# Kernel optimization log

Measured on AMD Instinct MI355X. Metric: run time of the kernel, lower is better.

Reference implementation:

```python
import jax, jax.numpy as jnp
import numpy as np

IN_SIZE = 64
RES = 1024
B = 16
T = 2048
ALPHA = 0.5
SPECTRAL_RADIUS = 0.9


def setup_inputs() -> dict:
    key = jax.random.key(0)
    ks = jax.random.split(key, 8)
    # W_hh scaled so spectral radius ~ SPECTRAL_RADIUS (circular law: |eig|max ~ sqrt(R)*std)
    scale_hh = SPECTRAL_RADIUS / np.sqrt(RES)
    return {
        "x": jax.random.normal(ks[0], (B, T, IN_SIZE), dtype=jnp.float32),
        "W_in0": jax.random.normal(ks[1], (IN_SIZE, RES), dtype=jnp.float32) * 0.5,
        "W_hh0": jax.random.normal(ks[2], (RES, RES), dtype=jnp.float32) * scale_hh,
        "b0": jax.random.normal(ks[3], (1, RES), dtype=jnp.float32) * 0.5,
        "W_in1": jax.random.normal(ks[4], (RES, RES), dtype=jnp.float32) * 0.1,
        "W_hh1": jax.random.normal(ks[5], (RES, RES), dtype=jnp.float32) * scale_hh,
        "b1": jax.random.normal(ks[6], (1, RES), dtype=jnp.float32) * 0.5,
        "readout": jax.random.normal(ks[7], (2 * RES, IN_SIZE), dtype=jnp.float32) * 0.02,
    }


def _reservoir_layer(xs, W_in, W_hh, b, alpha):
    # xs: [T, B, F] time-major; sequential leaky-integrator scan over T
    h0 = jnp.zeros((xs.shape[1], W_hh.shape[0]), dtype=xs.dtype)

    def step(h, x_i):
        h = (1.0 - alpha) * h + alpha * jnp.tanh(x_i @ W_in + h @ W_hh + b)
        return h, h

    _, states = jax.lax.scan(step, h0, xs)
    return states  # [T, B, R]


def reference(x, W_in0, W_hh0, b0, W_in1, W_hh1, b1, readout):
    xt = jnp.transpose(x, (1, 0, 2))  # [T, B, in]
    s0 = _reservoir_layer(xt, W_in0, W_hh0, b0, ALPHA)  # [T, B, R]
    s1 = _reservoir_layer(s0, W_in1, W_hh1, b1, ALPHA)  # [T, B, R]
    h = jnp.concatenate([s0, s1], axis=-1)  # [T, B, 2R]
    out = h @ readout  # [T, B, in]
    return jnp.transpose(out, (1, 0, 2))  # [B, T, in]
```

## Files before the change

### kernel.cpp

```cpp
#include <hip/hip_runtime.h>
#include <math.h>

#define ESN_B 16
#define ESN_T 2048
#define ESN_R 1024
#define ESN_IN 64
#define NBR (ESN_B * ESN_R)

#define OFF_WT_HH0 0
#define OFF_WT_IN1 (1024 * 1024)
#define OFF_WT_HH1 (2 * 1024 * 1024)
#define OFF_WT_IN0 (3 * 1024 * 1024)
#define OFF_RT     (OFF_WT_IN0 + 1024 * 64)
#define OFF_S0G    (OFF_RT + 64 * 2048)
#define OFF_S1G    (OFF_S0G + 2 * NBR)
#define OFF_FLAGS  (OFF_S1G + 2 * NBR)

typedef float vfloat4 __attribute__((__vector_size__(16)));

__global__ void __launch_bounds__(256) transpose_k(const float* __restrict__ src,
                                                   float* __restrict__ dst,
                                                   int rows, int cols) {
  __shared__ float tile[32][33];
  int bx = blockIdx.x * 32, by = blockIdx.y * 32;
  int tx = threadIdx.x, ty = threadIdx.y;
  #pragma unroll
  for (int i = ty; i < 32; i += 8) {
    int r = by + i, c = bx + tx;
    if (r < rows && c < cols) tile[i][tx] = src[(size_t)r * cols + c];
  }
  __syncthreads();
  #pragma unroll
  for (int i = ty; i < 32; i += 8) {
    int c = bx + i, r = by + tx;
    if (c < cols && r < rows) dst[(size_t)c * rows + r] = tile[tx][i];
  }
}

__device__ __forceinline__ float fast_tanh(float v) {
  float a = fabsf(v);
  float e = __expf(-2.0f * a);
  float t = __fdividef(1.0f - e, 1.0f + e);
  return copysignf(t, v);
}

__device__ __forceinline__ float dot4(float4 a, float4 b, float acc) {
  acc = fmaf(a.x, b.x, acc);
  acc = fmaf(a.y, b.y, acc);
  acc = fmaf(a.z, b.z, acc);
  acc = fmaf(a.w, b.w, acc);
  return acc;
}

__device__ __forceinline__ float wave_red64(float v) {
  #pragma unroll
  for (int off = 32; off > 0; off >>= 1) v += __shfl_xor(v, off, 64);
  return v;
}

__device__ __forceinline__ float reduce4(float a0, float a1, float a2, float a3,
                                         bool lb0, bool lb1) {
  float uA = lb0 ? a0 : a1, kA = lb0 ? a1 : a0;
  float A = kA + __shfl_xor(uA, 1, 64);
  float uB = lb0 ? a2 : a3, kB = lb0 ? a3 : a2;
  float B = kB + __shfl_xor(uB, 1, 64);
  float uC = lb1 ? A : B, kC = lb1 ? B : A;
  float C = kC + __shfl_xor(uC, 2, 64);
  C += __shfl_xor(C, 4, 64);
  C += __shfl_xor(C, 8, 64);
  C += __shfl_xor(C, 16, 64);
  C += __shfl_xor(C, 32, 64);
  return C;
}

__device__ __forceinline__ void llc_store_f32x4(float* p, float4 v) {
  vfloat4 vv = {v.x, v.y, v.z, v.w};
  asm volatile("global_store_dwordx4 %0, %1, off sc1" :: "v"(p), "v"(vv) : "memory");
}
__device__ __forceinline__ void llc_store_u32(unsigned* p, unsigned v) {
  asm volatile("global_store_dword %0, %1, off sc1" :: "v"(p), "v"(v) : "memory");
}
__device__ __forceinline__ unsigned llc_load_u32(const unsigned* p) {
  unsigned f;
  asm volatile("global_load_dword %0, %1, off sc1\n\ts_waitcnt vmcnt(0)"
               : "=v"(f) : "v"(p) : "memory");
  return f;
}
__device__ __forceinline__ void vmcnt0() {
  asm volatile("s_waitcnt vmcnt(0)" ::: "memory");
}
__device__ __forceinline__ void barrier_only() {
  asm volatile("" ::: "memory");
  __builtin_amdgcn_s_barrier();
  asm volatile("" ::: "memory");
}
__device__ __forceinline__ void barrier_lgkm() {
  asm volatile("s_waitcnt lgkmcnt(0)" ::: "memory");
  __builtin_amdgcn_s_barrier();
  asm volatile("" ::: "memory");
}

__global__ void __launch_bounds__(512, 2) esn_scan_kernel(
    const float* __restrict__ x,
    const float* __restrict__ b0,
    const float* __restrict__ b1,
    float* __restrict__ wsf,
    float* __restrict__ out) {
  __shared__ float s0l[2][4][1024];
  __shared__ float s1l[4][1024];
  __shared__ __align__(16) float res[2][4][16];
  extern __shared__ float dyn_pad[];
  if (blockIdx.x == 0x7fffffffu) dyn_pad[0] = 1.0f;

  const float* wtHH0 = wsf + OFF_WT_HH0;
  const float* wtIN1 = wsf + OFF_WT_IN1;
  const float* wtHH1 = wsf + OFF_WT_HH1;
  const float* wtIN0 = wsf + OFF_WT_IN0;
  const float* rt    = wsf + OFF_RT;
  float* s0g = wsf + OFF_S0G;
  float* s1g = wsf + OFF_S1G;
  unsigned* flags = (unsigned*)(wsf + OFF_FLAGS);

  const int tid = threadIdx.x;
  const int l = tid & 63;
  const int w = tid >> 6;
  const int bid = blockIdx.x;
  const int g = bid >> 6;
  const int bg = bid & 63;
  const int batch0 = g * 4;
  const int wg = bg * 8 + w;
  const int c0 = wg * 2;
  const int wl2 = w * 2;
  const bool doRO = (w >= 4);
  const int rbl = w - 4;
  const int rb = batch0 + rbl;
  const int roc = bg;
  unsigned* gflags = flags + g * 64;
  const bool lb0 = (l & 1) != 0;
  const bool lb1 = (l & 2) != 0;

  float4 wA0_0, wA0_1, wA0_2, wA0_3, wA1_0, wA1_1, wA1_2, wA1_3;
  float4 wB0_0, wB0_1, wB0_2, wB0_3, wB1_0, wB1_1, wB1_2, wB1_3;
  float4 wC0_0, wC0_1, wC0_2, wC0_3, wC1_0, wC1_1, wC1_2, wC1_3;
  float4 rd0, rd1, rd2, rd3, rd4, rd5, rd6, rd7;

#define LOADW(cc) { \
    const float* pA = wtHH0 + (size_t)(c0 + cc) * ESN_R + l * 4; \
    const float* pB = wtIN1 + (size_t)(c0 + cc) * ESN_R + l * 4; \
    const float* pC = wtHH1 + (size_t)(c0 + cc) * ESN_R + l * 4; \
    wA##cc##_0 = *(const float4*)(pA);       wA##cc##_1 = *(const float4*)(pA + 256); \
    wA##cc##_2 = *(const float4*)(pA + 512); wA##cc##_3 = *(const float4*)(pA + 768); \
    wB##cc##_0 = *(const float4*)(pB);       wB##cc##_1 = *(const float4*)(pB + 256); \
    wB##cc##_2 = *(const float4*)(pB + 512); wB##cc##_3 = *(const float4*)(pB + 768); \
    wC##cc##_0 = *(const float4*)(pC);       wC##cc##_1 = *(const float4*)(pC + 256); \
    wC##cc##_2 = *(const float4*)(pC + 512); wC##cc##_3 = *(const float4*)(pC + 768); \
  }
  LOADW(0) LOADW(1)
#undef LOADW

  rd0 = rd1 = rd2 = rd3 = rd4 = rd5 = rd6 = rd7 = make_float4(0.f, 0.f, 0.f, 0.f);
  if (doRO) {
    const float* pr = rt + (size_t)roc * 2048 + l * 4;
    rd0 = *(const float4*)(pr);        rd1 = *(const float4*)(pr + 256);
    rd2 = *(const float4*)(pr + 512);  rd3 = *(const float4*)(pr + 768);
    rd4 = *(const float4*)(pr + 1024); rd5 = *(const float4*)(pr + 1280);
    rd6 = *(const float4*)(pr + 1536); rd7 = *(const float4*)(pr + 1792);
  }
  const float wI0 = wtIN0[(size_t)(c0 + 0) * ESN_IN + l];
  const float wI1 = wtIN0[(size_t)(c0 + 1) * ESN_IN + l];
  float bsel = 0.f;
  if (l < 4) bsel = ((l < 2) ? b0 : b1)[c0 + (l & 1)];

  const float* sA0 = s0g + 0 * NBR + batch0 * ESN_R + tid * 4;
  const float* sA1 = s0g + 1 * NBR + batch0 * ESN_R + tid * 4;
  const float* sB0 = s1g + 0 * NBR + batch0 * ESN_R + tid * 4;
  const float* sB1 = s1g + 1 * NBR + batch0 * ESN_R + tid * 4;
  float* gb = ((l < 16) ? s0g : s1g) +
              (batch0 + ((l >> 2) & 3)) * ESN_R + bg * 16 + (l & 3) * 4;
  float* gbA = gb;
  float* gbB = gb + NBR;
  const float* xbase = x + (size_t)batch0 * ESN_T * ESN_IN + l;

#define ESN_ROUND(SLOTC, rr)                                                   \
  {                                                                            \
    const bool doL0 = ((rr) < ESN_T);                                          \
    const bool doL1 = ((rr) >= 1 && (rr) <= ESN_T);                            \
    float xv0 = 0.f, xv1 = 0.f, xv2 = 0.f, xv3 = 0.f;                          \
    if (doL0) {                                                                \
      const float* xp = xbase + (size_t)(rr) * ESN_IN;                         \
      xv0 = xp[0 * ESN_T * ESN_IN];                                            \
      xv1 = xp[1 * ESN_T * ESN_IN];                                            \
      xv2 = xp[2 * ESN_T * ESN_IN];                                            \
      xv3 = xp[3 * ESN_T * ESN_IN];                                            \
    }                                                                          \
    if ((rr) > 0) {                                                            \
      if (w == 0) {                                                            \
        while (!__all(llc_load_u32(&gflags[l]) >= (unsigned)(rr))) {}          \
      }                                                                        \
      barrier_only();            \
    }                                                                          \
    const float* p0 = SLOTC ? sA0 : sA1;        \
    const float* p1 = SLOTC ? sB0 : sB1;                                       \
    float4 t0, t1, u0, u1;                                                     \
    asm volatile(                                                              \
        "global_load_dwordx4 %0, %4, off sc1\n\t"                              \
        "global_load_dwordx4 %1, %5, off sc1\n\t"                              \
        "global_load_dwordx4 %2, %6, off sc1\n\t"                              \
        "global_load_dwordx4 %3, %7, off sc1\n\t"                              \
        "s_waitcnt vmcnt(0)"                                                   \
        : "=&v"(t0), "=&v"(t1), "=&v"(u0), "=&v"(u1)                           \
        : "v"(p0), "v"(p0 + 2048), "v"(p1), "v"(p1 + 2048)                     \
        : "memory");                                                           \
    {                                                                          \
      float* d0 = &s0l[SLOTC][0][0] + tid * 4;                                 \
      float* d1 = &s1l[0][0] + tid * 4;                                        \
      *(float4*)(d0)        = t0;                                              \
      *(float4*)(d0 + 2048) = t1;                                              \
      *(float4*)(d1)        = u0;                                              \
      *(float4*)(d1 + 2048) = u1;                                              \
    }                                                                          \
    barrier_lgkm();                                \
    _Pragma("unroll")                                                          \
    for (int bb = 0; bb < 4; ++bb) {                                           \
      const float* hp = &s0l[SLOTC][bb][l * 4];                                \
      float4 h0x = *(const float4*)(hp);                                       \
      float4 h1x = *(const float4*)(hp + 256);                                 \
      float4 h2x = *(const float4*)(hp + 512);                                 \
      float4 h3x = *(const float4*)(hp + 768);                                 \
      const float* gp = &s1l[bb][l * 4];                                       \
      float4 g0x = *(const float4*)(gp);                                       \
      float4 g1x = *(const float4*)(gp + 256);                                 \
      float4 g2x = *(const float4*)(gp + 512);                                 \
      float4 g3x = *(const float4*)(gp + 768);                                 \
      float xb = (bb == 0) ? xv0 : (bb == 1) ? xv1 : (bb == 2) ? xv2 : xv3;    \
      float a0 = xb * wI0, a1 = xb * wI1;                                      \
      a0 = dot4(wA0_0, h0x, a0); a0 = dot4(wA0_1, h1x, a0);                    \
      a0 = dot4(wA0_2, h2x, a0); a0 = dot4(wA0_3, h3x, a0);                    \
      a1 = dot4(wA1_0, h0x, a1); a1 = dot4(wA1_1, h1x, a1);                    \
      a1 = dot4(wA1_2, h2x, a1); a1 = dot4(wA1_3, h3x, a1);                    \
      float a2 = 0.f, a3 = 0.f;                                                \
      a2 = dot4(wB0_0, h0x, a2); a2 = dot4(wB0_1, h1x, a2);                    \
      a2 = dot4(wB0_2, h2x, a2); a2 = dot4(wB0_3, h3x, a2);                    \
      a2 = dot4(wC0_0, g0x, a2); a2 = dot4(wC0_1, g1x, a2);                    \
      a2 = dot4(wC0_2, g2x, a2); a2 = dot4(wC0_3, g3x, a2);                    \
      a3 = dot4(wB1_0, h0x, a3); a3 = dot4(wB1_1, h1x, a3);                    \
      a3 = dot4(wB1_2, h2x, a3); a3 = dot4(wB1_3, h3x, a3);                    \
      a3 = dot4(wC1_0, g0x, a3); a3 = dot4(wC1_1, g1x, a3);                    \
      a3 = dot4(wC1_2, g2x, a3); a3 = dot4(wC1_3, g3x, a3);                    \
      float C = reduce4(a0, a1, a2, a3, lb0, lb1);                             \
      if (l < 4) {                 \
        const float* pbase = (l < 2) ? &s0l[SLOTC][bb][0] : &s1l[bb][0];       \
        float prev = pbase[c0 + (l & 1)];                                      \
        float nv = 0.5f * prev + 0.5f * fast_tanh(C + bsel);                   \
        bool wr = (l < 2) ? doL0 : doL1;                                       \
        if (wr) res[l >> 1][bb][wl2 + (l & 1)] = nv;                           \
      }                                                                        \
    }                                                                          \
    barrier_lgkm();                                      \
    if (w == 0) {                                                              \
      if (l < 32 && ((l < 16) ? doL0 : doL1)) {                                \
        float4 v = *(const float4*)&res[l >> 4][(l >> 2) & 3][(l & 3) * 4];    \
        llc_store_f32x4(SLOTC ? gbB : gbA, v);                                 \
      }                                                                        \
      vmcnt0();                                                                \
      if (l == 0) llc_store_u32(&gflags[bg], (unsigned)((rr) + 1));            \
    }                                                                          \
    if ((rr) >= 2 && doRO) {                                                   \
      const float* sp = &s0l[1 - SLOTC][rbl][l * 4];                           \
      const float* tp = &s1l[rbl][l * 4];                                      \
      float a = 0.f;                                                           \
      a = dot4(rd0, *(const float4*)(sp), a);                                  \
      a = dot4(rd1, *(const float4*)(sp + 256), a);                            \
      a = dot4(rd2, *(const float4*)(sp + 512), a);                            \
      a = dot4(rd3, *(const float4*)(sp + 768), a);                            \
      a = dot4(rd4, *(const float4*)(tp), a);                                  \
      a = dot4(rd5, *(const float4*)(tp + 256), a);                            \
      a = dot4(rd6, *(const float4*)(tp + 512), a);                            \
      a = dot4(rd7, *(const float4*)(tp + 768), a);                            \
      a = wave_red64(a);                                                       \
      if (l == 0) out[((size_t)rb * ESN_T + ((rr) - 2)) * ESN_IN + roc] = a;   \
    }                                                                          \
  }

  for (int rp = 0; rp < (ESN_T + 2) / 2; ++rp) {
    const int r0 = rp * 2;
    ESN_ROUND(0, r0)
    ESN_ROUND(1, r0 + 1)
  }
#undef ESN_ROUND
}

extern "C" void kernel_launch(void* const* d_in, const int* in_sizes, int n_in,
                              void* d_out, int out_size, void* d_ws, size_t ws_size,
                              hipStream_t stream) {
  (void)in_sizes; (void)n_in; (void)out_size; (void)ws_size;
  const float* x     = (const float*)d_in[0];
  const float* w_in0 = (const float*)d_in[1];
  const float* w_hh0 = (const float*)d_in[2];
  const float* b0    = (const float*)d_in[3];
  const float* w_in1 = (const float*)d_in[4];
  const float* w_hh1 = (const float*)d_in[5];
  const float* b1    = (const float*)d_in[6];
  const float* rdo   = (const float*)d_in[7];
  float* out = (float*)d_out;
  float* wsf = (float*)d_ws;

  dim3 tb(32, 8);
  transpose_k<<<dim3(32, 32), tb, 0, stream>>>(w_hh0, wsf + OFF_WT_HH0, 1024, 1024);
  transpose_k<<<dim3(32, 32), tb, 0, stream>>>(w_in1, wsf + OFF_WT_IN1, 1024, 1024);
  transpose_k<<<dim3(32, 32), tb, 0, stream>>>(w_hh1, wsf + OFF_WT_HH1, 1024, 1024);
  transpose_k<<<dim3(32, 2),  tb, 0, stream>>>(w_in0, wsf + OFF_WT_IN0, 64, 1024);
  transpose_k<<<dim3(2, 64),  tb, 0, stream>>>(rdo,   wsf + OFF_RT, 2048, 64);

  (void)hipMemsetAsync(wsf + OFF_S0G + NBR, 0, NBR * sizeof(float), stream);
  (void)hipMemsetAsync(wsf + OFF_S1G, 0, 2 * NBR * sizeof(float), stream);
  (void)hipMemsetAsync(wsf + OFF_FLAGS, 0, 4 * 64 * sizeof(unsigned), stream);

  esn_scan_kernel<<<dim3(256), dim3(512), 40960, stream>>>(x, b0, b1, wsf, out);
}
```

Before: 11.48 ms.

## Triple-buffer layer-0 LDS state so every wave polls flags and one barrier is dropped

```diff
diff --git a/kernel.cpp b/kernel.cpp
--- a/kernel.cpp
+++ b/kernel.cpp
@@ -89,11 +89,6 @@
 __device__ __forceinline__ void vmcnt0() {
   asm volatile("s_waitcnt vmcnt(0)" ::: "memory");
 }
-__device__ __forceinline__ void barrier_only() {
-  asm volatile("" ::: "memory");
-  __builtin_amdgcn_s_barrier();
-  asm volatile("" ::: "memory");
-}
 __device__ __forceinline__ void barrier_lgkm() {
   asm volatile("s_waitcnt lgkmcnt(0)" ::: "memory");
   __builtin_amdgcn_s_barrier();
@@ -106,11 +101,9 @@
     const float* __restrict__ b1,
     float* __restrict__ wsf,
     float* __restrict__ out) {
-  __shared__ float s0l[2][4][1024];
-  __shared__ float s1l[4][1024];
-  __shared__ __align__(16) float res[2][4][16];
-  extern __shared__ float dyn_pad[];
-  if (blockIdx.x == 0x7fffffffu) dyn_pad[0] = 1.0f;
+  __shared__ float s0l[3][4][1024];
+  __shared__ float s1l[2][4][1024];
+  __shared__ __align__(16) float res[2][4][20];
 
   const float* wtHH0 = wsf + OFF_WT_HH0;
   const float* wtIN1 = wsf + OFF_WT_IN1;
@@ -131,7 +124,7 @@
   const int wg = bg * 8 + w;
   const int c0 = wg * 2;
   const int wl2 = w * 2;
-  const bool doRO = (w >= 4);
+  const bool doROw = (w >= 4);
   const int rbl = w - 4;
   const int rb = batch0 + rbl;
   const int roc = bg;
@@ -159,7 +152,7 @@
 #undef LOADW
 
   rd0 = rd1 = rd2 = rd3 = rd4 = rd5 = rd6 = rd7 = make_float4(0.f, 0.f, 0.f, 0.f);
-  if (doRO) {
+  if (doROw) {
     const float* pr = rt + (size_t)roc * 2048 + l * 4;
     rd0 = *(const float4*)(pr);        rd1 = *(const float4*)(pr + 256);
     rd2 = *(const float4*)(pr + 512);  rd3 = *(const float4*)(pr + 768);
@@ -181,10 +174,11 @@
   float* gbB = gb + NBR;
   const float* xbase = x + (size_t)batch0 * ESN_T * ESN_IN + l;
 
-#define ESN_ROUND(SLOTC, rr)                                                   \
+#define ESN_ROUND(S0S, PAR, rr)                                                \
   {                                                                            \
     const bool doL0 = ((rr) < ESN_T);                                          \
     const bool doL1 = ((rr) >= 1 && (rr) <= ESN_T);                            \
+    const bool doRO = ((rr) >= 2 && (rr) < ESN_T + 2) && doROw;                \
     float xv0 = 0.f, xv1 = 0.f, xv2 = 0.f, xv3 = 0.f;                          \
     if (doL0) {                                                                \
       const float* xp = xbase + (size_t)(rr) * ESN_IN;                         \
@@ -193,14 +187,11 @@
       xv2 = xp[2 * ESN_T * ESN_IN];                                            \
       xv3 = xp[3 * ESN_T * ESN_IN];                                            \
     }                                                                          \
-    if ((rr) > 0) {                                                            \
-      if (w == 0) {                                                            \
-        while (!__all(llc_load_u32(&gflags[l]) >= (unsigned)(rr))) {}          \
-      }                                                                        \
-      barrier_only();            \
-    }                                                                          \
-    const float* p0 = SLOTC ? sA0 : sA1;        \
-    const float* p1 = SLOTC ? sB0 : sB1;                                       \
+    if ((rr) > 0) {             \
+      while (!__all(llc_load_u32(&gflags[l]) >= (unsigned)(rr))) {}            \
+    }                                                                          \
+    const float* p0 = (PAR) ? sA0 : sA1;      \
+    const float* p1 = (PAR) ? sB0 : sB1;                                       \
     float4 t0, t1, u0, u1;                                                     \
     asm volatile(                                                              \
         "global_load_dwordx4 %0, %4, off sc1\n\t"                              \
@@ -212,22 +203,22 @@
         : "v"(p0), "v"(p0 + 2048), "v"(p1), "v"(p1 + 2048)                     \
         : "memory");                                                           \
     {                                                                          \
-      float* d0 = &s0l[SLOTC][0][0] + tid * 4;                                 \
-      float* d1 = &s1l[0][0] + tid * 4;                                        \
+      float* d0 = &s0l[S0S][0][0] + tid * 4;                                   \
+      float* d1 = &s1l[PAR][0][0] + tid * 4;                                   \
       *(float4*)(d0)        = t0;                                              \
       *(float4*)(d0 + 2048) = t1;                                              \
       *(float4*)(d1)        = u0;                                              \
       *(float4*)(d1 + 2048) = u1;                                              \
     }                                                                          \
-    barrier_lgkm();                                \
+    barrier_lgkm();                     \
     _Pragma("unroll")                                                          \
     for (int bb = 0; bb < 4; ++bb) {                                           \
-      const float* hp = &s0l[SLOTC][bb][l * 4];                                \
+      const float* hp = &s0l[S0S][bb][l * 4];                                  \
       float4 h0x = *(const float4*)(hp);                                       \
       float4 h1x = *(const float4*)(hp + 256);                                 \
       float4 h2x = *(const float4*)(hp + 512);                                 \
       float4 h3x = *(const float4*)(hp + 768);                                 \
-      const float* gp = &s1l[bb][l * 4];                                       \
+      const float* gp = &s1l[PAR][bb][l * 4];                                  \
       float4 g0x = *(const float4*)(gp);                                       \
       float4 g1x = *(const float4*)(gp + 256);                                 \
       float4 g2x = *(const float4*)(gp + 512);                                 \
@@ -249,7 +240,7 @@
       a3 = dot4(wC1_2, g2x, a3); a3 = dot4(wC1_3, g3x, a3);                    \
       float C = reduce4(a0, a1, a2, a3, lb0, lb1);                             \
       if (l < 4) {                 \
-        const float* pbase = (l < 2) ? &s0l[SLOTC][bb][0] : &s1l[bb][0];       \
+        const float* pbase = (l < 2) ? &s0l[S0S][bb][0] : &s1l[PAR][bb][0];    \
         float prev = pbase[c0 + (l & 1)];                                      \
         float nv = 0.5f * prev + 0.5f * fast_tanh(C + bsel);                   \
         bool wr = (l < 2) ? doL0 : doL1;                                       \
@@ -259,15 +250,19 @@
     barrier_lgkm();                                      \
     if (w == 0) {                                                              \
       if (l < 32 && ((l < 16) ? doL0 : doL1)) {                                \
-        float4 v = *(const float4*)&res[l >> 4][(l >> 2) & 3][(l & 3) * 4];    \
-        llc_store_f32x4(SLOTC ? gbB : gbA, v);                                 \
+        float4 v;                                                              \
+        {                                                                      \
+          const float* rp_ = &res[l >> 4][(l >> 2) & 3][(l & 3) * 4];          \
+          v = *(const float4*)rp_;                                             \
+        }                                                                      \
+        llc_store_f32x4((PAR) ? gbB : gbA, v);                                 \
       }                                                                        \
       vmcnt0();                                                                \
       if (l == 0) llc_store_u32(&gflags[bg], (unsigned)((rr) + 1));            \
     }                                                                          \
-    if ((rr) >= 2 && doRO) {                                                   \
-      const float* sp = &s0l[1 - SLOTC][rbl][l * 4];                           \
-      const float* tp = &s1l[rbl][l * 4];                                      \
+    if (doRO) {   \
+      const float* sp = &s0l[(S0S + 2) % 3][rbl][l * 4];                       \
+      const float* tp = &s1l[PAR][rbl][l * 4];                                 \
       float a = 0.f;                                                           \
       a = dot4(rd0, *(const float4*)(sp), a);                                  \
       a = dot4(rd1, *(const float4*)(sp + 256), a);                            \
@@ -282,10 +277,14 @@
     }                                                                          \
   }
 
-  for (int rp = 0; rp < (ESN_T + 2) / 2; ++rp) {
-    const int r0 = rp * 2;
-    ESN_ROUND(0, r0)
-    ESN_ROUND(1, r0 + 1)
+  for (int rp = 0; rp < 342; ++rp) {
+    const int r0 = rp * 6;
+    ESN_ROUND(0, 0, r0 + 0)
+    ESN_ROUND(1, 1, r0 + 1)
+    ESN_ROUND(2, 0, r0 + 2)
+    ESN_ROUND(0, 1, r0 + 3)
+    ESN_ROUND(1, 0, r0 + 4)
+    ESN_ROUND(2, 1, r0 + 5)
   }
 #undef ESN_ROUND
 }
@@ -316,5 +315,5 @@
   (void)hipMemsetAsync(wsf + OFF_S1G, 0, 2 * NBR * sizeof(float), stream);
   (void)hipMemsetAsync(wsf + OFF_FLAGS, 0, 4 * 64 * sizeof(unsigned), stream);
 
-  esn_scan_kernel<<<dim3(256), dim3(512), 40960, stream>>>(x, b0, b1, wsf, out);
-}
+  esn_scan_kernel<<<dim3(256), dim3(512), 0, stream>>>(x, b0, b1, wsf, out);
+}
```

Measured after the change: 14.55 ms. +26.8%, slower.

## Publish per-wave state and flags directly, dropping block-level staging barrier

Applied to the files above, without the earlier changes.

```diff
diff --git a/kernel.cpp b/kernel.cpp
--- a/kernel.cpp
+++ b/kernel.cpp
@@ -6,6 +6,7 @@
 #define ESN_R 1024
 #define ESN_IN 64
 #define NBR (ESN_B * ESN_R)
+#define SLOTF 16384
 
 #define OFF_WT_HH0 0
 #define OFF_WT_IN1 (1024 * 1024)
@@ -13,8 +14,8 @@
 #define OFF_WT_IN0 (3 * 1024 * 1024)
 #define OFF_RT     (OFF_WT_IN0 + 1024 * 64)
 #define OFF_S0G    (OFF_RT + 64 * 2048)
-#define OFF_S1G    (OFF_S0G + 2 * NBR)
-#define OFF_FLAGS  (OFF_S1G + 2 * NBR)
+#define OFF_S1G    (OFF_S0G + 2 * SLOTF)
+#define OFF_FLAGS  (OFF_S1G + 2 * SLOTF)
 
 typedef float vfloat4 __attribute__((__vector_size__(16)));
 
@@ -73,18 +74,8 @@
   return C;
 }
 
-__device__ __forceinline__ void llc_store_f32x4(float* p, float4 v) {
-  vfloat4 vv = {v.x, v.y, v.z, v.w};
-  asm volatile("global_store_dwordx4 %0, %1, off sc1" :: "v"(p), "v"(vv) : "memory");
-}
 __device__ __forceinline__ void llc_store_u32(unsigned* p, unsigned v) {
   asm volatile("global_store_dword %0, %1, off sc1" :: "v"(p), "v"(v) : "memory");
-}
-__device__ __forceinline__ unsigned llc_load_u32(const unsigned* p) {
-  unsigned f;
-  asm volatile("global_load_dword %0, %1, off sc1\n\ts_waitcnt vmcnt(0)"
-               : "=v"(f) : "v"(p) : "memory");
-  return f;
 }
 __device__ __forceinline__ void vmcnt0() {
   asm volatile("s_waitcnt vmcnt(0)" ::: "memory");
@@ -108,7 +99,6 @@
     float* __restrict__ out) {
   __shared__ float s0l[2][4][1024];
   __shared__ float s1l[4][1024];
-  __shared__ __align__(16) float res[2][4][16];
   extern __shared__ float dyn_pad[];
   if (blockIdx.x == 0x7fffffffu) dyn_pad[0] = 1.0f;
 
@@ -130,12 +120,12 @@
   const int batch0 = g * 4;
   const int wg = bg * 8 + w;
   const int c0 = wg * 2;
-  const int wl2 = w * 2;
-  const bool doRO = (w >= 4);
+  const bool doROw = (w >= 4);
   const int rbl = w - 4;
   const int rb = batch0 + rbl;
   const int roc = bg;
-  unsigned* gflags = flags + g * 64;
+  unsigned* gflags = flags + g * 512;
+  unsigned* myflag = gflags + bg * 8 + w;
   const bool lb0 = (l & 1) != 0;
   const bool lb1 = (l & 2) != 0;
 
@@ -159,7 +149,7 @@
 #undef LOADW
 
   rd0 = rd1 = rd2 = rd3 = rd4 = rd5 = rd6 = rd7 = make_float4(0.f, 0.f, 0.f, 0.f);
-  if (doRO) {
+  if (doROw) {
     const float* pr = rt + (size_t)roc * 2048 + l * 4;
     rd0 = *(const float4*)(pr);        rd1 = *(const float4*)(pr + 256);
     rd2 = *(const float4*)(pr + 512);  rd3 = *(const float4*)(pr + 768);
@@ -171,20 +161,20 @@
   float bsel = 0.f;
   if (l < 4) bsel = ((l < 2) ? b0 : b1)[c0 + (l & 1)];
 
-  const float* sA0 = s0g + 0 * NBR + batch0 * ESN_R + tid * 4;
-  const float* sA1 = s0g + 1 * NBR + batch0 * ESN_R + tid * 4;
-  const float* sB0 = s1g + 0 * NBR + batch0 * ESN_R + tid * 4;
-  const float* sB1 = s1g + 1 * NBR + batch0 * ESN_R + tid * 4;
-  float* gb = ((l < 16) ? s0g : s1g) +
-              (batch0 + ((l >> 2) & 3)) * ESN_R + bg * 16 + (l & 3) * 4;
-  float* gbA = gb;
-  float* gbB = gb + NBR;
+  const float* sA0 = s0g + 0 * SLOTF + g * 4096 + tid * 4;
+  const float* sA1 = s0g + 1 * SLOTF + g * 4096 + tid * 4;
+  const float* sB0 = s1g + 0 * SLOTF + g * 4096 + tid * 4;
+  const float* sB1 = s1g + 1 * SLOTF + g * 4096 + tid * 4;
+  float* stv = ((l < 2) ? s0g : s1g) + g * 4096 + (c0 + (l & 1)) * 4;
+  float* stA = stv;
+  float* stB = stv + SLOTF;
   const float* xbase = x + (size_t)batch0 * ESN_T * ESN_IN + l;
 
-#define ESN_ROUND(SLOTC, rr)                                                   \
+#define ESN_ROUND(PAR, rr)                                                     \
   {                                                                            \
     const bool doL0 = ((rr) < ESN_T);                                          \
     const bool doL1 = ((rr) >= 1 && (rr) <= ESN_T);                            \
+    const bool doRO = ((rr) >= 2) && doROw;                                    \
     float xv0 = 0.f, xv1 = 0.f, xv2 = 0.f, xv3 = 0.f;                          \
     if (doL0) {                                                                \
       const float* xp = xbase + (size_t)(rr) * ESN_IN;                         \
@@ -194,13 +184,26 @@
       xv3 = xp[3 * ESN_T * ESN_IN];                                            \
     }                                                                          \
     if ((rr) > 0) {                                                            \
-      if (w == 0) {                                                            \
-        while (!__all(llc_load_u32(&gflags[l]) >= (unsigned)(rr))) {}          \
+      if (w == 0) {            \
+        const unsigned* fp = gflags + l * 8;                                   \
+        for (;;) {                                                             \
+          uint4 fa, fb;                                                        \
+          asm volatile(                                                        \
+              "global_load_dwordx4 %0, %2, off sc1\n\t"                        \
+              "global_load_dwordx4 %1, %3, off sc1\n\t"                        \
+              "s_waitcnt vmcnt(0)"                                             \
+              : "=&v"(fa), "=&v"(fb) : "v"(fp), "v"(fp + 4) : "memory");       \
+          bool ok = fa.x >= (unsigned)(rr) && fa.y >= (unsigned)(rr) &&        \
+                    fa.z >= (unsigned)(rr) && fa.w >= (unsigned)(rr) &&        \
+                    fb.x >= (unsigned)(rr) && fb.y >= (unsigned)(rr) &&        \
+                    fb.z >= (unsigned)(rr) && fb.w >= (unsigned)(rr);          \
+          if (__all(ok)) break;                                                \
+        }                                                                      \
       }                                                                        \
-      barrier_only();            \
-    }                                                                          \
-    const float* p0 = SLOTC ? sA0 : sA1;        \
-    const float* p1 = SLOTC ? sB0 : sB1;                                       \
+      barrier_only();                                               \
+    }                                                                          \
+    const float* q0 = (PAR) ? sA0 : sA1;                  \
+    const float* q1 = (PAR) ? sB0 : sB1;                                       \
     float4 t0, t1, u0, u1;                                                     \
     asm volatile(                                                              \
         "global_load_dwordx4 %0, %4, off sc1\n\t"                              \
@@ -209,20 +212,21 @@
         "global_load_dwordx4 %3, %7, off sc1\n\t"                              \
         "s_waitcnt vmcnt(0)"                                                   \
         : "=&v"(t0), "=&v"(t1), "=&v"(u0), "=&v"(u1)                           \
-        : "v"(p0), "v"(p0 + 2048), "v"(p1), "v"(p1 + 2048)                     \
+        : "v"(q0), "v"(q0 + 2048), "v"(q1), "v"(q1 + 2048)                     \
         : "memory");                                                           \
-    {                                                                          \
-      float* d0 = &s0l[SLOTC][0][0] + tid * 4;                                 \
-      float* d1 = &s1l[0][0] + tid * 4;                                        \
-      *(float4*)(d0)        = t0;                                              \
-      *(float4*)(d0 + 2048) = t1;                                              \
-      *(float4*)(d1)        = u0;                                              \
-      *(float4*)(d1 + 2048) = u1;                                              \
-    }                                                                          \
-    barrier_lgkm();                                \
+    {     \
+      float* d0 = &s0l[PAR][0][0] + tid;                                       \
+      d0[0] = t0.x; d0[1024] = t0.y; d0[2048] = t0.z; d0[3072] = t0.w;         \
+      d0[512] = t1.x; d0[1536] = t1.y; d0[2560] = t1.z; d0[3584] = t1.w;       \
+      float* d1 = &s1l[0][0] + tid;                                            \
+      d1[0] = u0.x; d1[1024] = u0.y; d1[2048] = u0.z; d1[3072] = u0.w;         \
+      d1[512] = u1.x; d1[1536] = u1.y; d1[2560] = u1.z; d1[3584] = u1.w;       \
+    }                                                                          \
+    barrier_lgkm();                          \
+    float rv0 = 0.f, rv1 = 0.f, rv2 = 0.f, rv3 = 0.f;                          \
     _Pragma("unroll")                                                          \
     for (int bb = 0; bb < 4; ++bb) {                                           \
-      const float* hp = &s0l[SLOTC][bb][l * 4];                                \
+      const float* hp = &s0l[PAR][bb][l * 4];                                  \
       float4 h0x = *(const float4*)(hp);                                       \
       float4 h1x = *(const float4*)(hp + 256);                                 \
       float4 h2x = *(const float4*)(hp + 512);                                 \
@@ -249,24 +253,26 @@
       a3 = dot4(wC1_2, g2x, a3); a3 = dot4(wC1_3, g3x, a3);                    \
       float C = reduce4(a0, a1, a2, a3, lb0, lb1);                             \
       if (l < 4) {                 \
-        const float* pbase = (l < 2) ? &s0l[SLOTC][bb][0] : &s1l[bb][0];       \
+        const float* pbase = (l < 2) ? &s0l[PAR][bb][0] : &s1l[bb][0];         \
         float prev = pbase[c0 + (l & 1)];                                      \
         float nv = 0.5f * prev + 0.5f * fast_tanh(C + bsel);                   \
-        bool wr = (l < 2) ? doL0 : doL1;                                       \
-        if (wr) res[l >> 1][bb][wl2 + (l & 1)] = nv;                           \
+        if (bb == 0) rv0 = nv; else if (bb == 1) rv1 = nv;                     \
+        else if (bb == 2) rv2 = nv; else rv3 = nv;                             \
       }                                                                        \
     }                                                                          \
-    barrier_lgkm();                                      \
-    if (w == 0) {                                                              \
-      if (l < 32 && ((l < 16) ? doL0 : doL1)) {                                \
-        float4 v = *(const float4*)&res[l >> 4][(l >> 2) & 3][(l & 3) * 4];    \
-        llc_store_f32x4(SLOTC ? gbB : gbA, v);                                 \
+    {                \
+      bool wrv = (l < 4) && ((l < 2) ? doL0 : doL1);                           \
+      if (wrv) {                                                               \
+        vfloat4 vv = {rv0, rv1, rv2, rv3};                                     \
+        float* sp_ = (PAR) ? stB : stA;                  \
+        asm volatile("global_store_dwordx4 %0, %1, off sc1"                    \
+                     :: "v"(sp_), "v"(vv) : "memory");                         \
       }                                                                        \
-      vmcnt0();                                                                \
-      if (l == 0) llc_store_u32(&gflags[bg], (unsigned)((rr) + 1));            \
-    }                                                                          \
-    if ((rr) >= 2 && doRO) {                                                   \
-      const float* sp = &s0l[1 - SLOTC][rbl][l * 4];                           \
+    }                                                                          \
+    vmcnt0();                                            \
+    if (l == 0) llc_store_u32(myflag, (unsigned)((rr) + 1));                   \
+    if (doRO) {                \
+      const float* sp = &s0l[1 - (PAR)][rbl][l * 4];                           \
       const float* tp = &s1l[rbl][l * 4];                                      \
       float a = 0.f;                                                           \
       a = dot4(rd0, *(const float4*)(sp), a);                                  \
@@ -312,9 +318,9 @@
   transpose_k<<<dim3(32, 2),  tb, 0, stream>>>(w_in0, wsf + OFF_WT_IN0, 64, 1024);
   transpose_k<<<dim3(2, 64),  tb, 0, stream>>>(rdo,   wsf + OFF_RT, 2048, 64);
 
-  (void)hipMemsetAsync(wsf + OFF_S0G + NBR, 0, NBR * sizeof(float), stream);
-  (void)hipMemsetAsync(wsf + OFF_S1G, 0, 2 * NBR * sizeof(float), stream);
-  (void)hipMemsetAsync(wsf + OFF_FLAGS, 0, 4 * 64 * sizeof(unsigned), stream);
+  (void)hipMemsetAsync(wsf + OFF_S0G + SLOTF, 0, SLOTF * sizeof(float), stream);
+  (void)hipMemsetAsync(wsf + OFF_S1G, 0, 2 * SLOTF * sizeof(float), stream);
+  (void)hipMemsetAsync(wsf + OFF_FLAGS, 0, 4 * 512 * sizeof(unsigned), stream);
 
   esn_scan_kernel<<<dim3(256), dim3(512), 40960, stream>>>(x, b0, b1, wsf, out);
 }
```

New measurement: 12.99 ms. 1.13x slower.
